# Performance work log

Measured on AMD Instinct MI355X. Metric: run time of the kernel, lower is better.

The kernel has to match this reference:

```python
import jax, jax.numpy as jnp
import numpy as np

D_IN = 1024
D_OUT = 1024
D_BOT = 512


def setup_inputs() -> dict:
    key = jax.random.key(0)
    ks = jax.random.split(key, 16)
    B, Sq, Skv = 8, 2048, 2048

    def lin(k, fan_in, fan_out):
        kw, kb = jax.random.split(k)
        bound = 1.0 / np.sqrt(fan_in)
        W = jax.random.uniform(kw, (fan_in, fan_out), jnp.float32, -bound, bound)
        b = jax.random.uniform(kb, (fan_out,), jnp.float32, -bound, bound)
        return W, b

    W1, b1 = lin(ks[0], D_IN, D_IN)
    W2, b2 = lin(ks[1], D_IN, D_BOT)
    W3, b3 = lin(ks[2], D_BOT, D_IN)
    W4, b4 = lin(ks[3], D_IN, D_IN)
    Wq, bq = lin(ks[4], D_IN, D_OUT)
    Wk, bk = lin(ks[5], D_IN, D_OUT)
    Wv, bv = lin(ks[6], D_IN, D_OUT)

    x = jax.random.normal(ks[7], (B, Sq, D_IN), jnp.float32)
    y = jax.random.normal(ks[8], (B, Skv, D_IN), jnp.float32)
    return {
        "x": x, "y": y,
        "W1": W1, "b1": b1, "W2": W2, "b2": b2,
        "W3": W3, "b3": b3, "W4": W4, "b4": b4,
        "Wq": Wq, "bq": bq, "Wk": Wk, "bk": bk, "Wv": Wv, "bv": bv,
    }


def reference(x, y, W1, b1, W2, b2, W3, b3, W4, b4, Wq, bq, Wk, bk, Wv, bv):
    # 4-layer MLP with ReLU after every linear
    h = jax.nn.relu(x @ W1 + b1)
    h = jax.nn.relu(h @ W2 + b2)
    h = jax.nn.relu(h @ W3 + b3)
    h = jax.nn.relu(h @ W4 + b4)
    # cross-attention projections
    q = h @ Wq + bq          # [B, Sq, D_OUT]
    k = y @ Wk + bk          # [B, Skv, D_OUT]
    v = y @ Wv + bv          # [B, Skv, D_OUT]
    scale = 1.0 / jnp.sqrt(jnp.float32(q.shape[-1]))
    scores = jnp.einsum('bqd,bkd->bqk', q, k) * scale  # [B, Sq, Skv]
    attn_w = jax.nn.softmax(scores, axis=-1)
    out = jnp.einsum('bqk,bkd->bqd', attn_w, v)
    return out
```

## Files before the change

### kernel.cpp

```cpp
#include <hip/hip_runtime.h>
#include <stdint.h>


typedef __attribute__((ext_vector_type(8))) short bf16x8;
typedef __attribute__((ext_vector_type(4))) float f32x4;
typedef __attribute__((ext_vector_type(8))) unsigned short u16x8;

__device__ __forceinline__ float bf2f(unsigned short u) {
    return __uint_as_float(((unsigned int)u) << 16);
}
__device__ __forceinline__ unsigned short f2bf(float f) {
    unsigned int u = __float_as_uint(f);
    unsigned int r = (u + 0x7fffu + ((u >> 16) & 1u)) >> 16;
    return (unsigned short)r;
}

__device__ __forceinline__ void async16(const void* g, void* l) {
    __builtin_amdgcn_global_load_lds(
        (const __attribute__((address_space(1))) unsigned int*)g,
        (__attribute__((address_space(3))) unsigned int*)l,
        16, 0, 0);
}

__global__ __launch_bounds__(64) void detect_dtype(
    const unsigned short* __restrict__ w, int* __restrict__ flag)
{
    const int t = threadIdx.x;
    int cnt = 0;
    for (int i = t; i < 4096; i += 64) {
        const unsigned e = (w[i] >> 7) & 0xFF;
        cnt += (e >= 140) ? 1 : 0;
    }
#pragma unroll
    for (int off = 32; off; off >>= 1) cnt += __shfl_xor(cnt, off, 64);
    if (t == 0) flag[0] = (cnt >= 8) ? 1 : 0;
}

__global__ __launch_bounds__(256) void conv_bias_all(
    const void* b1, const void* b2, const void* b3, const void* b4,
    const void* bq, const void* bk, const void* bv,
    float* __restrict__ out, const int* __restrict__ flag)
{
    const int i = blockIdx.x * 256 + threadIdx.x;
    const int slot = i >> 10, idx = i & 1023;
    if (slot == 1 && idx >= 512) return;
    const void* src = (slot == 0) ? b1 : (slot == 1) ? b2 : (slot == 2) ? b3 :
                      (slot == 3) ? b4 : (slot == 4) ? bq : (slot == 5) ? bk : bv;
    out[i] = (*flag) ? ((const float*)src)[idx]
                     : bf2f(((const unsigned short*)src)[idx]);
}

__device__ __forceinline__ void wt_body(
    const void* in, unsigned short* out, int R, int C, int f)
{
    __shared__ unsigned short tile[32][33];
    const int bc = blockIdx.x * 32;
    const int br = blockIdx.y * 32;
    const int x = threadIdx.x & 31;
    const int y = threadIdx.x >> 5;
#pragma unroll
    for (int i = 0; i < 4; i++) {
        const int r = y + i * 8;
        unsigned short v;
        if (f) v = f2bf(((const float*)in)[(size_t)(br + r) * C + bc + x]);
        else   v = ((const unsigned short*)in)[(size_t)(br + r) * C + bc + x];
        tile[r][x] = v;
    }
    __syncthreads();
#pragma unroll
    for (int i = 0; i < 4; i++) {
        const int r = y + i * 8;
        out[(size_t)(bc + r) * R + br + x] = tile[x][r];
    }
}

__global__ __launch_bounds__(256) void conv_weight_t7(
    const void* i0, unsigned short* o0, const void* i1, unsigned short* o1,
    const void* i2, unsigned short* o2, const void* i3, unsigned short* o3,
    const void* i4, unsigned short* o4, const void* i5, unsigned short* o5,
    const void* i6, unsigned short* o6, const int* flag)
{
    const int z = blockIdx.z;
    if (z == 5) {
        if (blockIdx.x >= 16) return;
        wt_body(i5, o5, 1024, 512, *flag);
        return;
    }
    if (z == 6) {
        if (blockIdx.y >= 16) return;
        wt_body(i6, o6, 512, 1024, *flag);
        return;
    }
    const void* in = (z == 0) ? i0 : (z == 1) ? i1 : (z == 2) ? i2 : (z == 3) ? i3 : i4;
    unsigned short* out = (z == 0) ? o0 : (z == 1) ? o1 : (z == 2) ? o2 : (z == 3) ? o3 : o4;
    wt_body(in, out, 1024, 1024, *flag);
}

__global__ __launch_bounds__(256) void conv_to_bf16(
    const void* __restrict__ in, unsigned short* __restrict__ out,
    int n, const int* __restrict__ flag)
{
    const int i = (blockIdx.x * 256 + threadIdx.x) * 8;
    if (i >= n) return;
    if (*flag) {
        const float4* p = (const float4*)((const float*)in + i);
        const float4 a = p[0], b = p[1];
        u16x8 o;
        o[0] = f2bf(a.x); o[1] = f2bf(a.y); o[2] = f2bf(a.z); o[3] = f2bf(a.w);
        o[4] = f2bf(b.x); o[5] = f2bf(b.y); o[6] = f2bf(b.z); o[7] = f2bf(b.w);
        *(u16x8*)(out + i) = o;
    } else {
        *(u16x8*)(out + i) = *(const u16x8*)((const unsigned short*)in + i);
    }
}

__global__ __launch_bounds__(256) void write_out(
    const unsigned short* __restrict__ src, void* __restrict__ dst,
    int n, const int* __restrict__ flag)
{
    const int i = (blockIdx.x * 256 + threadIdx.x) * 8;
    if (i >= n) return;
    const u16x8 v = *(const u16x8*)(src + i);
    if (*flag) {
        float4 a, b;
        a.x = bf2f(v[0]); a.y = bf2f(v[1]); a.z = bf2f(v[2]); a.w = bf2f(v[3]);
        b.x = bf2f(v[4]); b.y = bf2f(v[5]); b.z = bf2f(v[6]); b.w = bf2f(v[7]);
        float4* p = (float4*)((float*)dst + i);
        p[0] = a; p[1] = b;
    } else {
        *(u16x8*)((unsigned short*)dst + i) = v;
    }
}

template <int RELU, int BIAS, int OUTF, int SWZ>
__global__ __launch_bounds__(256, 2) void gemm_bt(
    const unsigned short* __restrict__ A, const unsigned short* __restrict__ B,
    const float* __restrict__ bias, void* __restrict__ C,
    int M, int N, int K, float alpha,
    long long sA, long long sB, long long sC, const int* __restrict__ flag)
{
    int bxi = blockIdx.x, byi = blockIdx.y;
    if (SWZ) {
        const int id = byi * gridDim.x + bxi;
        bxi = (id >> 3) % gridDim.x;
        byi = (id >> 3) / gridDim.x * 8 + (id & 7);
    }
    const int z = blockIdx.z;
    A += (size_t)z * (size_t)sA;
    B += (size_t)z * (size_t)sB;
    const size_t cofs = (size_t)z * (size_t)sC;

    const int bm = byi * 128;
    const int bn = bxi * 128;
    const int t = threadIdx.x;
    const int lane = t & 63;
    const int w = t >> 6;
    const int wr = (w >> 1) * 64;
    const int wc = (w & 1) * 64;

    __shared__ unsigned short sAt[128 * 32];
    __shared__ unsigned short sBt[128 * 32];

    f32x4 acc[4][4];
#pragma unroll
    for (int i = 0; i < 4; i++)
#pragma unroll
        for (int j = 0; j < 4; j++)
            acc[i][j] = (f32x4){0.f, 0.f, 0.f, 0.f};

    const int tr = t >> 2;
    const int tc = (t & 3) << 3;
    const unsigned short* ga = A + (size_t)(bm + tr) * K + tc;
    const unsigned short* gb = B + (size_t)(bn + tr) * K + tc;
    unsigned short* la = &sAt[tr * 32 + tc];
    unsigned short* lb = &sBt[tr * 32 + tc];

    const int am = wr + (lane & 15);
    const int bn_ = wc + (lane & 15);
    const int ak = (lane >> 4) * 8;

    for (int k0 = 0; k0 < K; k0 += 32) {
        async16(ga, la);
        async16(ga + (size_t)64 * K, la + 64 * 32);
        async16(gb, lb);
        async16(gb + (size_t)64 * K, lb + 64 * 32);
        ga += 32;
        gb += 32;
        __syncthreads();

        bf16x8 af[4], bfr[4];
#pragma unroll
        for (int i = 0; i < 4; i++)
            af[i] = *(const bf16x8*)&sAt[(am + i * 16) * 32 + ak];
#pragma unroll
        for (int j = 0; j < 4; j++)
            bfr[j] = *(const bf16x8*)&sBt[(bn_ + j * 16) * 32 + ak];
#pragma unroll
        for (int i = 0; i < 4; i++)
#pragma unroll
            for (int j = 0; j < 4; j++)
                acc[i][j] = __builtin_amdgcn_mfma_f32_16x16x32_bf16(
                    af[i], bfr[j], acc[i][j], 0, 0, 0);
        __syncthreads();
    }

    const int fl = OUTF ? *flag : 0;
#pragma unroll
    for (int i = 0; i < 4; i++) {
        const int row0 = bm + wr + i * 16 + (lane >> 4) * 4;
#pragma unroll
        for (int j = 0; j < 4; j++) {
            const int col = bn + wc + j * 16 + (lane & 15);
            float bc = 0.f;
            if (BIAS == 1) bc = bias[col];
#pragma unroll
            for (int r = 0; r < 4; r++) {
                float bv = bc;
                if (BIAS == 2) bv = bias[row0 + r];
                float vv = acc[i][j][r] * alpha + bv;
                if (RELU) vv = fmaxf(vv, 0.f);
                const size_t idx = cofs + (size_t)(row0 + r) * N + col;
                if (OUTF && fl) ((float*)C)[idx] = vv;
                else ((unsigned short*)C)[idx] = f2bf(vv);
            }
        }
    }
}

template <int RELU, int BIAS, int OUTF, int SWZ>
__global__ __launch_bounds__(256, 2) void gemm_bt2(
    const unsigned short* __restrict__ A, const unsigned short* __restrict__ B,
    const float* __restrict__ bias, void* __restrict__ C,
    int M, int N, int K, float alpha,
    long long sA, long long sB, long long sC, const int* __restrict__ flag)
{
    int bxi = blockIdx.x, byi = blockIdx.y;
    if (SWZ) {
        const int id = byi * gridDim.x + bxi;
        bxi = (id >> 3) % gridDim.x;
        byi = (id >> 3) / gridDim.x * 8 + (id & 7);
    }
    const int z = blockIdx.z;
    A += (size_t)z * (size_t)sA;
    B += (size_t)z * (size_t)sB;
    const size_t cofs = (size_t)z * (size_t)sC;

    const int bm = byi * 128;
    const int bn = bxi * 256;
    const int t = threadIdx.x;
    const int lane = t & 63;
    const int w = t >> 6;
    const int wr = (w >> 1) * 64;
    const int wc = (w & 1) * 128;

    __shared__ unsigned short sAt[128 * 32];
    __shared__ unsigned short sBt[256 * 32];

    f32x4 acc[4][8];
#pragma unroll
    for (int i = 0; i < 4; i++)
#pragma unroll
        for (int j = 0; j < 8; j++)
            acc[i][j] = (f32x4){0.f, 0.f, 0.f, 0.f};

    const int tr = t >> 2;
    const int tc = (t & 3) << 3;
    const unsigned short* ga = A + (size_t)(bm + tr) * K + tc;
    const unsigned short* gb = B + (size_t)(bn + tr) * K + tc;
    unsigned short* la = &sAt[tr * 32 + tc];
    unsigned short* lb = &sBt[tr * 32 + tc];

    const int am = wr + (lane & 15);
    const int bn_ = wc + (lane & 15);
    const int ak = (lane >> 4) * 8;

    for (int k0 = 0; k0 < K; k0 += 32) {
        async16(ga, la);
        async16(ga + (size_t)64 * K, la + 64 * 32);
        async16(gb, lb);
        async16(gb + (size_t)64 * K, lb + 64 * 32);
        async16(gb + (size_t)128 * K, lb + 128 * 32);
        async16(gb + (size_t)192 * K, lb + 192 * 32);
        ga += 32;
        gb += 32;
        __syncthreads();

        bf16x8 af[4], bfr[8];
#pragma unroll
        for (int i = 0; i < 4; i++)
            af[i] = *(const bf16x8*)&sAt[(am + i * 16) * 32 + ak];
#pragma unroll
        for (int j = 0; j < 8; j++)
            bfr[j] = *(const bf16x8*)&sBt[(bn_ + j * 16) * 32 + ak];
#pragma unroll
        for (int i = 0; i < 4; i++)
#pragma unroll
            for (int j = 0; j < 8; j++)
                acc[i][j] = __builtin_amdgcn_mfma_f32_16x16x32_bf16(
                    af[i], bfr[j], acc[i][j], 0, 0, 0);
        __syncthreads();
    }

    const int fl = OUTF ? *flag : 0;
#pragma unroll
    for (int i = 0; i < 4; i++) {
        const int row0 = bm + wr + i * 16 + (lane >> 4) * 4;
#pragma unroll
        for (int j = 0; j < 8; j++) {
            const int col = bn + wc + j * 16 + (lane & 15);
            float bc = 0.f;
            if (BIAS == 1) bc = bias[col];
#pragma unroll
            for (int r = 0; r < 4; r++) {
                float bv = bc;
                if (BIAS == 2) bv = bias[row0 + r];
                float vv = acc[i][j][r] * alpha + bv;
                if (RELU) vv = fmaxf(vv, 0.f);
                const size_t idx = cofs + (size_t)(row0 + r) * N + col;
                if (OUTF && fl) ((float*)C)[idx] = vv;
                else ((unsigned short*)C)[idx] = f2bf(vv);
            }
        }
    }
}

__global__ __launch_bounds__(256) void softmax_rows(unsigned short* S, int n)
{
    const size_t row = blockIdx.x;
    unsigned short* p = S + row * (size_t)n;
    const int t = threadIdx.x;
    const int lane = t & 63;
    const int wave = t >> 6;

    u16x8 v = *(const u16x8*)(p + t * 8);
    float f[8];
    float m = -3.0e38f;
#pragma unroll
    for (int i = 0; i < 8; i++) {
        f[i] = bf2f(v[i]);
        m = fmaxf(m, f[i]);
    }
#pragma unroll
    for (int off = 32; off; off >>= 1) m = fmaxf(m, __shfl_xor(m, off, 64));
    __shared__ float redm[4];
    if (lane == 0) redm[wave] = m;
    __syncthreads();
    m = fmaxf(fmaxf(redm[0], redm[1]), fmaxf(redm[2], redm[3]));

    float e[8];
    float s = 0.f;
#pragma unroll
    for (int i = 0; i < 8; i++) {
        e[i] = __expf(f[i] - m);
        s += e[i];
    }
#pragma unroll
    for (int off = 32; off; off >>= 1) s += __shfl_xor(s, off, 64);
    __shared__ float reds[4];
    if (lane == 0) reds[wave] = s;
    __syncthreads();
    s = reds[0] + reds[1] + reds[2] + reds[3];
    const float inv = 1.0f / s;

    u16x8 o;
#pragma unroll
    for (int i = 0; i < 8; i++) o[i] = f2bf(e[i] * inv);
    *(u16x8*)(p + t * 8) = o;
}

extern "C" void kernel_launch(void* const* d_in, const int* in_sizes, int n_in,
                              void* d_out, int out_size, void* d_ws, size_t ws_size,
                              hipStream_t stream)
{
    const void* x  = d_in[0];
    const void* y  = d_in[1];
    const void* W1 = d_in[2];
    const void* b1 = d_in[3];
    const void* W2 = d_in[4];
    const void* b2 = d_in[5];
    const void* W3 = d_in[6];
    const void* b3 = d_in[7];
    const void* W4 = d_in[8];
    const void* b4 = d_in[9];
    const void* Wq = d_in[10];
    const void* bq = d_in[11];
    const void* Wk = d_in[12];
    const void* bk = d_in[13];
    const void* Wv = d_in[14];
    const void* bv = d_in[15];

    int* flag = (int*)d_ws;
    float* fb = (float*)((char*)d_ws + 64);
    unsigned short* arena = (unsigned short*)((char*)d_ws + 64 + 7 * 1024 * 4);
    const size_t baseB = 64 + 7 * 1024 * 4;
    const size_t MEG = 1024ull * 1024ull;

    auto needB = [&](int G, bool direct) -> size_t {
        return baseB + 2ull * ((6 + 16 + (size_t)G * 6 + (direct ? 0 : 16)) * MEG);
    };
    int G; bool direct;
    if (ws_size >= needB(8, true))      { G = 8; direct = true;  }
    else if (ws_size >= needB(4, false)) { G = 4; direct = false; }
    else if (ws_size >= needB(2, false)) { G = 2; direct = false; }
    else                                 { G = 1; direct = false; }

    unsigned short* W1t = arena;
    unsigned short* W2t = W1t + 1 * MEG;
    unsigned short* W3t = W2t + MEG / 2;
    unsigned short* W4t = W3t + MEG / 2;
    unsigned short* Wqt = W4t + 1 * MEG;
    unsigned short* Wkt = Wqt + 1 * MEG;
    unsigned short* Wvt = Wkt + 1 * MEG;
    unsigned short* XC  = Wvt + 1 * MEG;
    unsigned short* VT  = XC + 16 * MEG;
    unsigned short* SBUF = VT + (size_t)G * 2 * MEG;
    unsigned short* OUTS = SBUF + (size_t)G * 4 * MEG;

    unsigned short* PA = (unsigned short*)d_out;
    unsigned short* PB = PA + 16 * MEG;

    float* fb1 = fb;
    float* fb2 = fb + 1024;
    float* fb3 = fb + 2048;
    float* fb4 = fb + 3072;
    float* fbq = fb + 4096;
    float* fbk = fb + 5120;
    float* fbv = fb + 6144;

    const dim3 blk(256);
    const int NE = 16 * 1024 * 1024;
    const int Mx = 16384;
    const long long Z0 = 0;
    const long long sQK = 2048ll * 1024;
    const long long sS  = 2048ll * 2048;

    detect_dtype<<<1, 64, 0, stream>>>((const unsigned short*)W1, flag);
    conv_bias_all<<<28, blk, 0, stream>>>(b1, b2, b3, b4, bq, bk, bv, fb, flag);
    conv_weight_t7<<<dim3(32, 32, 7), blk, 0, stream>>>(
        W1, W1t, W4, W4t, Wq, Wqt, Wk, Wkt, Wv, Wvt, W2, W2t, W3, W3t, flag);

    conv_to_bf16<<<8192, blk, 0, stream>>>(x, XC, NE, flag);

    gemm_bt2<1, 1, 0, 1><<<dim3(4, 128), blk, 0, stream>>>(XC, W1t, fb1, PA, Mx, 1024, 1024, 1.f, Z0, Z0, Z0, flag);
    gemm_bt <1, 1, 0, 1><<<dim3(4, 128), blk, 0, stream>>>(PA, W2t, fb2, PB, Mx, 512, 1024, 1.f, Z0, Z0, Z0, flag);
    gemm_bt <1, 1, 0, 1><<<dim3(8, 128), blk, 0, stream>>>(PB, W3t, fb3, PA, Mx, 1024, 512, 1.f, Z0, Z0, Z0, flag);
    gemm_bt2<1, 1, 0, 1><<<dim3(4, 128), blk, 0, stream>>>(PA, W4t, fb4, PB, Mx, 1024, 1024, 1.f, Z0, Z0, Z0, flag);

    gemm_bt2<0, 1, 0, 1><<<dim3(4, 128), blk, 0, stream>>>(PB, Wqt, fbq, PA, Mx, 1024, 1024, 1.f, Z0, Z0, Z0, flag);
    conv_to_bf16<<<8192, blk, 0, stream>>>(y, XC, NE, flag);
    gemm_bt2<0, 1, 0, 1><<<dim3(4, 128), blk, 0, stream>>>(XC, Wkt, fbk, PB, Mx, 1024, 1024, 1.f, Z0, Z0, Z0, flag);

    if (direct) {
        gemm_bt<0, 2, 0, 0><<<dim3(16, 8, 8), blk, 0, stream>>>(
            Wvt, XC, fbv, VT, 1024, 2048, 1024, 1.f, Z0, sQK, sQK, flag);
        gemm_bt2<0, 0, 0, 1><<<dim3(8, 16, 8), blk, 0, stream>>>(
            PA, PB, nullptr, SBUF, 2048, 2048, 1024, 0.03125f, sQK, sQK, sS, flag);
        softmax_rows<<<dim3(8 * 2048), blk, 0, stream>>>(SBUF, 2048);
        gemm_bt2<0, 0, 1, 1><<<dim3(4, 16, 8), blk, 0, stream>>>(
            SBUF, VT, nullptr, d_out, 2048, 1024, 2048, 1.f, sS, sQK, sQK, flag);
    } else {
        for (int g = 0; g < 8; g += G) {
            const size_t off = (size_t)g * 2048 * 1024;
            gemm_bt<0, 2, 0, 0><<<dim3(16, 8, G), blk, 0, stream>>>(
                Wvt, XC + off, fbv, VT, 1024, 2048, 1024, 1.f, Z0, sQK, sQK, flag);
            gemm_bt<0, 0, 0, 1><<<dim3(16, 16, G), blk, 0, stream>>>(
                PA + off, PB + off, nullptr, SBUF, 2048, 2048, 1024, 0.03125f, sQK, sQK, sS, flag);
            softmax_rows<<<dim3(G * 2048), blk, 0, stream>>>(SBUF, 2048);
            gemm_bt<0, 0, 0, 1><<<dim3(8, 16, G), blk, 0, stream>>>(
                SBUF, VT, nullptr, OUTS + off, 2048, 1024, 2048, 1.f, sS, sQK, sQK, flag);
        }
        write_out<<<8192, blk, 0, stream>>>(OUTS, d_out, NE, flag);
    }
}
```

Baseline: 666.5 us.

## Replace 128x256 GEMM with 256x256 eight-wave double-buffered pipelined kernel

```diff
diff --git a/kernel.cpp b/kernel.cpp
--- a/kernel.cpp
+++ b/kernel.cpp
@@ -227,13 +227,76 @@
     }
 }
 
+#define G8_STG(gbase, dbase, T, h) do {                                        \
+    const unsigned short* _s = (gbase) + (size_t)((h) * 128) * K               \
+                                       + (size_t)(T) * 64;                     \
+    unsigned short* _d = (dbase) + (((T) & 1) ? 16384 : 0) + (h) * 8192;       \
+    async16(_s, _d);                                                           \
+    async16(_s + (size_t)64 * K, _d + 4096);                                   \
+} while (0)
+
+#define G8_RD_LO(PA_, PB_)                                                     \
+    _Pragma("unroll")                                                          \
+    for (int m_ = 0; m_ < 4; m_++) {                                           \
+        aL[m_][0] = *(const bf16x8*)&(PA_)[rA + m_ * 1024 + c0];               \
+        aL[m_][1] = *(const bf16x8*)&(PA_)[rA + m_ * 1024 + c1];               \
+    }                                                                          \
+    _Pragma("unroll")                                                          \
+    for (int n_ = 0; n_ < 4; n_++)                                             \
+        bb[n_][0] = *(const bf16x8*)&(PB_)[rB + n_ * 1024 + c0];
+
+#define G8_RD_HI(PA_, PB_)                                                     \
+    _Pragma("unroll")                                                          \
+    for (int m_ = 0; m_ < 4; m_++) {                                           \
+        aH[m_][0] = *(const bf16x8*)&(PA_)[rA + (m_ + 4) * 1024 + c0];         \
+        aH[m_][1] = *(const bf16x8*)&(PA_)[rA + (m_ + 4) * 1024 + c1];         \
+    }                                                                          \
+    _Pragma("unroll")                                                          \
+    for (int n_ = 0; n_ < 4; n_++)                                             \
+        bb[n_][1] = *(const bf16x8*)&(PB_)[rB + n_ * 1024 + c1];
+
+#define G8_TOP()                                                               \
+    __builtin_amdgcn_s_barrier();                                              \
+    asm volatile("s_waitcnt lgkmcnt(0)" ::: "memory");                         \
+    __builtin_amdgcn_sched_barrier(0);                                         \
+    __builtin_amdgcn_s_setprio(1);
+
+#define G8_FMA(AF, KK, MOFS)                                                   \
+    _Pragma("unroll")                                                          \
+    for (int m_ = 0; m_ < 4; m_++) {                                           \
+        _Pragma("unroll")                                                      \
+        for (int n_ = 0; n_ < 4; n_++)                                         \
+            acc[(MOFS) + m_][n_] = __builtin_amdgcn_mfma_f32_16x16x32_bf16(    \
+                AF[m_][KK], bb[n_][KK], acc[(MOFS) + m_][n_], 0, 0, 0);        \
+    }
+
+#define G8_BOT()                                                               \
+    __builtin_amdgcn_s_setprio(0);                                             \
+    asm volatile("" ::: "memory");                                             \
+    __builtin_amdgcn_s_barrier();                                              \
+    asm volatile("" ::: "memory");
+
+#define G8_BOTVM4()                                                            \
+    __builtin_amdgcn_s_setprio(0);                                             \
+    asm volatile("s_waitcnt vmcnt(4)" ::: "memory");                           \
+    __builtin_amdgcn_s_barrier();                                              \
+    asm volatile("" ::: "memory");
+
+#define G8_BOTVM0()                                                            \
+    __builtin_amdgcn_s_setprio(0);                                             \
+    asm volatile("s_waitcnt vmcnt(0)" ::: "memory");                           \
+    __builtin_amdgcn_s_barrier();                                              \
+    asm volatile("" ::: "memory");
+
 template <int RELU, int BIAS, int OUTF, int SWZ>
-__global__ __launch_bounds__(256, 2) void gemm_bt2(
+__global__ __launch_bounds__(512, 2) void gemm8(
     const unsigned short* __restrict__ A, const unsigned short* __restrict__ B,
     const float* __restrict__ bias, void* __restrict__ C,
     int M, int N, int K, float alpha,
     long long sA, long long sB, long long sC, const int* __restrict__ flag)
 {
+    extern __shared__ unsigned short lds[];
+    (void)M;
     int bxi = blockIdx.x, byi = blockIdx.y;
     if (SWZ) {
         const int id = byi * gridDim.x + bxi;
@@ -245,76 +308,136 @@
     B += (size_t)z * (size_t)sB;
     const size_t cofs = (size_t)z * (size_t)sC;
 
-    const int bm = byi * 128;
+    const int bm = byi * 256;
     const int bn = bxi * 256;
     const int t = threadIdx.x;
     const int lane = t & 63;
     const int w = t >> 6;
-    const int wr = (w >> 1) * 64;
-    const int wc = (w & 1) * 128;
-
-    __shared__ unsigned short sAt[128 * 32];
-    __shared__ unsigned short sBt[256 * 32];
-
-    f32x4 acc[4][8];
-#pragma unroll
-    for (int i = 0; i < 4; i++)
-#pragma unroll
-        for (int j = 0; j < 8; j++)
+    const int wm = w >> 2;
+    const int wn = w & 3;
+
+    unsigned short* LA = lds;
+    unsigned short* LB = lds + 32768;
+
+    const int rowi = t >> 3;
+    const int co = ((t & 7) ^ (rowi & 7)) << 3;
+    const unsigned short* gA = A + (size_t)(bm + rowi) * K + co;
+    const unsigned short* gB = B + (size_t)(bn + rowi) * K + co;
+    unsigned short* dA = LA + t * 8;
+    unsigned short* dB = LB + t * 8;
+
+    const int rA = (wm * 128 + (lane & 15)) * 64;
+    const int rB = (wn * 64 + (lane & 15)) * 64;
+    const int swz = (lane & 7) << 4;
+    const int c0 = ((((lane >> 4) << 4)) ^ swz) >> 1;
+    const int c1 = ((64 | ((lane >> 4) << 4)) ^ swz) >> 1;
+
+    f32x4 acc[8][4];
+#pragma unroll
+    for (int i = 0; i < 8; i++)
+#pragma unroll
+        for (int j = 0; j < 4; j++)
             acc[i][j] = (f32x4){0.f, 0.f, 0.f, 0.f};
 
-    const int tr = t >> 2;
-    const int tc = (t & 3) << 3;
-    const unsigned short* ga = A + (size_t)(bm + tr) * K + tc;
-    const unsigned short* gb = B + (size_t)(bn + tr) * K + tc;
-    unsigned short* la = &sAt[tr * 32 + tc];
-    unsigned short* lb = &sBt[tr * 32 + tc];
-
-    const int am = wr + (lane & 15);
-    const int bn_ = wc + (lane & 15);
-    const int ak = (lane >> 4) * 8;
-
-    for (int k0 = 0; k0 < K; k0 += 32) {
-        async16(ga, la);
-        async16(ga + (size_t)64 * K, la + 64 * 32);
-        async16(gb, lb);
-        async16(gb + (size_t)64 * K, lb + 64 * 32);
-        async16(gb + (size_t)128 * K, lb + 128 * 32);
-        async16(gb + (size_t)192 * K, lb + 192 * 32);
-        ga += 32;
-        gb += 32;
-        __syncthreads();
-
-        bf16x8 af[4], bfr[8];
-#pragma unroll
-        for (int i = 0; i < 4; i++)
-            af[i] = *(const bf16x8*)&sAt[(am + i * 16) * 32 + ak];
-#pragma unroll
-        for (int j = 0; j < 8; j++)
-            bfr[j] = *(const bf16x8*)&sBt[(bn_ + j * 16) * 32 + ak];
-#pragma unroll
-        for (int i = 0; i < 4; i++)
-#pragma unroll
-            for (int j = 0; j < 8; j++)
-                acc[i][j] = __builtin_amdgcn_mfma_f32_16x16x32_bf16(
-                    af[i], bfr[j], acc[i][j], 0, 0, 0);
-        __syncthreads();
+    bf16x8 aL[4][2], aH[4][2], bb[4][2];
+
+    G8_STG(gA, dA, 0, 0);
+    G8_STG(gA, dA, 0, 1);
+    G8_STG(gB, dB, 0, 0);
+    G8_STG(gB, dB, 0, 1);
+    G8_STG(gA, dA, 1, 0);
+    G8_STG(gA, dA, 1, 1);
+    asm volatile("s_waitcnt vmcnt(4)" ::: "memory");
+    __builtin_amdgcn_s_barrier();
+    asm volatile("" ::: "memory");
+
+    const int NI = K >> 7;
+    int kt = 0;
+    for (int i = 0; i < NI - 1; ++i, kt += 2) {
+        G8_RD_LO(LA, LB)
+        G8_STG(gB, dB, kt + 1, 0);
+        G8_TOP()
+        G8_FMA(aL, 0, 0)
+        G8_BOT()
+        G8_RD_HI(LA, LB)
+        G8_STG(gB, dB, kt + 1, 1);
+        G8_TOP()
+        G8_FMA(aL, 1, 0)
+        G8_BOT()
+        G8_STG(gA, dA, kt + 2, 0);
+        G8_TOP()
+        G8_FMA(aH, 0, 4)
+        G8_BOT()
+        G8_STG(gA, dA, kt + 2, 1);
+        G8_TOP()
+        G8_FMA(aH, 1, 4)
+        G8_BOTVM4()
+        G8_RD_LO((LA + 16384), (LB + 16384))
+        G8_STG(gB, dB, kt + 2, 0);
+        G8_TOP()
+        G8_FMA(aL, 0, 0)
+        G8_BOT()
+        G8_RD_HI((LA + 16384), (LB + 16384))
+        G8_STG(gB, dB, kt + 2, 1);
+        G8_TOP()
+        G8_FMA(aL, 1, 0)
+        G8_BOT()
+        G8_STG(gA, dA, kt + 3, 0);
+        G8_TOP()
+        G8_FMA(aH, 0, 4)
+        G8_BOT()
+        G8_STG(gA, dA, kt + 3, 1);
+        G8_TOP()
+        G8_FMA(aH, 1, 4)
+        G8_BOTVM4()
+    }
+    {
+        G8_RD_LO(LA, LB)
+        G8_STG(gB, dB, kt + 1, 0);
+        G8_TOP()
+        G8_FMA(aL, 0, 0)
+        G8_BOT()
+        G8_RD_HI(LA, LB)
+        G8_STG(gB, dB, kt + 1, 1);
+        G8_TOP()
+        G8_FMA(aL, 1, 0)
+        G8_BOT()
+        G8_TOP()
+        G8_FMA(aH, 0, 4)
+        G8_BOT()
+        G8_TOP()
+        G8_FMA(aH, 1, 4)
+        G8_BOTVM0()
+        G8_RD_LO((LA + 16384), (LB + 16384))
+        G8_TOP()
+        G8_FMA(aL, 0, 0)
+        G8_BOT()
+        G8_RD_HI((LA + 16384), (LB + 16384))
+        G8_TOP()
+        G8_FMA(aL, 1, 0)
+        G8_BOT()
+        G8_TOP()
+        G8_FMA(aH, 0, 4)
+        G8_BOT()
+        G8_TOP()
+        G8_FMA(aH, 1, 4)
+        __builtin_amdgcn_s_setprio(0);
     }
 
     const int fl = OUTF ? *flag : 0;
 #pragma unroll
-    for (int i = 0; i < 4; i++) {
-        const int row0 = bm + wr + i * 16 + (lane >> 4) * 4;
-#pragma unroll
-        for (int j = 0; j < 8; j++) {
-            const int col = bn + wc + j * 16 + (lane & 15);
+    for (int mi = 0; mi < 8; mi++) {
+        const int row0 = bm + wm * 128 + mi * 16 + (lane >> 4) * 4;
+#pragma unroll
+        for (int n = 0; n < 4; n++) {
+            const int col = bn + wn * 64 + n * 16 + (lane & 15);
             float bc = 0.f;
             if (BIAS == 1) bc = bias[col];
 #pragma unroll
             for (int r = 0; r < 4; r++) {
                 float bv = bc;
                 if (BIAS == 2) bv = bias[row0 + r];
-                float vv = acc[i][j][r] * alpha + bv;
+                float vv = acc[mi][n][r] * alpha + bv;
                 if (RELU) vv = fmaxf(vv, 0.f);
                 const size_t idx = cofs + (size_t)(row0 + r) * N + col;
                 if (OUTF && fl) ((float*)C)[idx] = vv;
@@ -428,12 +551,25 @@
     float* fbv = fb + 6144;
 
     const dim3 blk(256);
+    const dim3 blk8(512);
+    const int LDS8 = 131072;
     const int NE = 16 * 1024 * 1024;
     const int Mx = 16384;
     const long long Z0 = 0;
     const long long sQK = 2048ll * 1024;
     const long long sS  = 2048ll * 2048;
 
+    (void)hipFuncSetAttribute((const void*)&gemm8<1, 1, 0, 1>,
+                              hipFuncAttributeMaxDynamicSharedMemorySize, LDS8);
+    (void)hipFuncSetAttribute((const void*)&gemm8<0, 1, 0, 1>,
+                              hipFuncAttributeMaxDynamicSharedMemorySize, LDS8);
+    (void)hipFuncSetAttribute((const void*)&gemm8<0, 2, 0, 0>,
+                              hipFuncAttributeMaxDynamicSharedMemorySize, LDS8);
+    (void)hipFuncSetAttribute((const void*)&gemm8<0, 0, 0, 1>,
+                              hipFuncAttributeMaxDynamicSharedMemorySize, LDS8);
+    (void)hipFuncSetAttribute((const void*)&gemm8<0, 0, 1, 1>,
+                              hipFuncAttributeMaxDynamicSharedMemorySize, LDS8);
+
     detect_dtype<<<1, 64, 0, stream>>>((const unsigned short*)W1, flag);
     conv_bias_all<<<28, blk, 0, stream>>>(b1, b2, b3, b4, bq, bk, bv, fb, flag);
     conv_weight_t7<<<dim3(32, 32, 7), blk, 0, stream>>>(
@@ -441,22 +577,28 @@
 
     conv_to_bf16<<<8192, blk, 0, stream>>>(x, XC, NE, flag);
 
-    gemm_bt2<1, 1, 0, 1><<<dim3(4, 128), blk, 0, stream>>>(XC, W1t, fb1, PA, Mx, 1024, 1024, 1.f, Z0, Z0, Z0, flag);
-    gemm_bt <1, 1, 0, 1><<<dim3(4, 128), blk, 0, stream>>>(PA, W2t, fb2, PB, Mx, 512, 1024, 1.f, Z0, Z0, Z0, flag);
-    gemm_bt <1, 1, 0, 1><<<dim3(8, 128), blk, 0, stream>>>(PB, W3t, fb3, PA, Mx, 1024, 512, 1.f, Z0, Z0, Z0, flag);
-    gemm_bt2<1, 1, 0, 1><<<dim3(4, 128), blk, 0, stream>>>(PA, W4t, fb4, PB, Mx, 1024, 1024, 1.f, Z0, Z0, Z0, flag);
-
-    gemm_bt2<0, 1, 0, 1><<<dim3(4, 128), blk, 0, stream>>>(PB, Wqt, fbq, PA, Mx, 1024, 1024, 1.f, Z0, Z0, Z0, flag);
+    gemm8<1, 1, 0, 1><<<dim3(4, 64), blk8, LDS8, stream>>>(
+        XC, W1t, fb1, PA, Mx, 1024, 1024, 1.f, Z0, Z0, Z0, flag);
+    gemm_bt<1, 1, 0, 1><<<dim3(4, 128), blk, 0, stream>>>(
+        PA, W2t, fb2, PB, Mx, 512, 1024, 1.f, Z0, Z0, Z0, flag);
+    gemm8<1, 1, 0, 1><<<dim3(4, 64), blk8, LDS8, stream>>>(
+        PB, W3t, fb3, PA, Mx, 1024, 512, 1.f, Z0, Z0, Z0, flag);
+    gemm8<1, 1, 0, 1><<<dim3(4, 64), blk8, LDS8, stream>>>(
+        PA, W4t, fb4, PB, Mx, 1024, 1024, 1.f, Z0, Z0, Z0, flag);
+
+    gemm8<0, 1, 0, 1><<<dim3(4, 64), blk8, LDS8, stream>>>(
+        PB, Wqt, fbq, PA, Mx, 1024, 1024, 1.f, Z0, Z0, Z0, flag);
     conv_to_bf16<<<8192, blk, 0, stream>>>(y, XC, NE, flag);
-    gemm_bt2<0, 1, 0, 1><<<dim3(4, 128), blk, 0, stream>>>(XC, Wkt, fbk, PB, Mx, 1024, 1024, 1.f, Z0, Z0, Z0, flag);
+    gemm8<0, 1, 0, 1><<<dim3(4, 64), blk8, LDS8, stream>>>(
+        XC, Wkt, fbk, PB, Mx, 1024, 1024, 1.f, Z0, Z0, Z0, flag);
 
     if (direct) {
-        gemm_bt<0, 2, 0, 0><<<dim3(16, 8, 8), blk, 0, stream>>>(
+        gemm8<0, 2, 0, 0><<<dim3(8, 4, 8), blk8, LDS8, stream>>>(
             Wvt, XC, fbv, VT, 1024, 2048, 1024, 1.f, Z0, sQK, sQK, flag);
-        gemm_bt2<0, 0, 0, 1><<<dim3(8, 16, 8), blk, 0, stream>>>(
+        gemm8<0, 0, 0, 1><<<dim3(8, 8, 8), blk8, LDS8, stream>>>(
             PA, PB, nullptr, SBUF, 2048, 2048, 1024, 0.03125f, sQK, sQK, sS, flag);
         softmax_rows<<<dim3(8 * 2048), blk, 0, stream>>>(SBUF, 2048);
-        gemm_bt2<0, 0, 1, 1><<<dim3(4, 16, 8), blk, 0, stream>>>(
+        gemm8<0, 0, 1, 1><<<dim3(4, 8, 8), blk8, LDS8, stream>>>(
             SBUF, VT, nullptr, d_out, 2048, 1024, 2048, 1.f, sS, sQK, sQK, flag);
     } else {
         for (int g = 0; g < 8; g += G) {
```

Result: faster. 621.1 us (-6.8%).

## Replace GEMM kernel with 256x256 tile, 8-wave, 4-stage async LDS pipeline

Applied to the files above, without the earlier changes.

```diff
diff --git a/kernel.cpp b/kernel.cpp
--- a/kernel.cpp
+++ b/kernel.cpp
@@ -227,13 +227,22 @@
     }
 }
 
+#define G10_STG(SOFS, KOFS) do {                                               \
+    async16(gAs + (KOFS), dA + (SOFS));                                        \
+    async16(gAs + (KOFS) + rk128, dA + (SOFS) + 4096);                         \
+    async16(gBs + (KOFS), dB + (SOFS));                                        \
+    async16(gBs + (KOFS) + rk128, dB + (SOFS) + 4096);                         \
+} while (0)
+
 template <int RELU, int BIAS, int OUTF, int SWZ>
-__global__ __launch_bounds__(256, 2) void gemm_bt2(
+__global__ __launch_bounds__(512, 2) void gemm8(
     const unsigned short* __restrict__ A, const unsigned short* __restrict__ B,
     const float* __restrict__ bias, void* __restrict__ C,
     int M, int N, int K, float alpha,
     long long sA, long long sB, long long sC, const int* __restrict__ flag)
 {
+    extern __shared__ unsigned short lds[];
+    (void)M;
     int bxi = blockIdx.x, byi = blockIdx.y;
     if (SWZ) {
         const int id = byi * gridDim.x + bxi;
@@ -245,76 +254,89 @@
     B += (size_t)z * (size_t)sB;
     const size_t cofs = (size_t)z * (size_t)sC;
 
-    const int bm = byi * 128;
+    const int bm = byi * 256;
     const int bn = bxi * 256;
     const int t = threadIdx.x;
     const int lane = t & 63;
     const int w = t >> 6;
-    const int wr = (w >> 1) * 64;
-    const int wc = (w & 1) * 128;
-
-    __shared__ unsigned short sAt[128 * 32];
-    __shared__ unsigned short sBt[256 * 32];
-
-    f32x4 acc[4][8];
-#pragma unroll
-    for (int i = 0; i < 4; i++)
-#pragma unroll
-        for (int j = 0; j < 8; j++)
+    const int wm = w >> 2;
+    const int wn = w & 3;
+
+    const int soct = ((t & 3) ^ ((t >> 3) & 3)) << 3;
+    const unsigned short* gAs = A + (size_t)(bm + (t >> 2)) * K + soct;
+    const unsigned short* gBs = B + (size_t)(bn + (t >> 2)) * K + soct;
+    const size_t rk128 = (size_t)128 * K;
+    unsigned short* dA = lds + t * 8;
+    unsigned short* dB = lds + 32768 + t * 8;
+
+    const int l15 = lane & 15;
+    const int oct = (((lane >> 4) ^ ((lane >> 1) & 3)) << 3);
+    const int aoff = (wm * 128 + l15) * 32 + oct;
+    const int boff = (wn * 64 + l15) * 32 + oct;
+
+    f32x4 acc[8][4];
+#pragma unroll
+    for (int i = 0; i < 8; i++)
+#pragma unroll
+        for (int j = 0; j < 4; j++)
             acc[i][j] = (f32x4){0.f, 0.f, 0.f, 0.f};
 
-    const int tr = t >> 2;
-    const int tc = (t & 3) << 3;
-    const unsigned short* ga = A + (size_t)(bm + tr) * K + tc;
-    const unsigned short* gb = B + (size_t)(bn + tr) * K + tc;
-    unsigned short* la = &sAt[tr * 32 + tc];
-    unsigned short* lb = &sBt[tr * 32 + tc];
-
-    const int am = wr + (lane & 15);
-    const int bn_ = wc + (lane & 15);
-    const int ak = (lane >> 4) * 8;
-
-    for (int k0 = 0; k0 < K; k0 += 32) {
-        async16(ga, la);
-        async16(ga + (size_t)64 * K, la + 64 * 32);
-        async16(gb, lb);
-        async16(gb + (size_t)64 * K, lb + 64 * 32);
-        async16(gb + (size_t)128 * K, lb + 128 * 32);
-        async16(gb + (size_t)192 * K, lb + 192 * 32);
-        ga += 32;
-        gb += 32;
-        __syncthreads();
-
-        bf16x8 af[4], bfr[8];
-#pragma unroll
-        for (int i = 0; i < 4; i++)
-            af[i] = *(const bf16x8*)&sAt[(am + i * 16) * 32 + ak];
-#pragma unroll
-        for (int j = 0; j < 8; j++)
-            bfr[j] = *(const bf16x8*)&sBt[(bn_ + j * 16) * 32 + ak];
-#pragma unroll
-        for (int i = 0; i < 4; i++)
-#pragma unroll
-            for (int j = 0; j < 8; j++)
-                acc[i][j] = __builtin_amdgcn_mfma_f32_16x16x32_bf16(
-                    af[i], bfr[j], acc[i][j], 0, 0, 0);
-        __syncthreads();
+    G10_STG(0, 0);
+    G10_STG(8192, 32);
+    asm volatile("s_waitcnt vmcnt(4)" ::: "memory");
+    __builtin_amdgcn_s_barrier();
+    asm volatile("" ::: "memory");
+
+    const int NT = K >> 5;
+    for (int T = 0; T < NT; ++T) {
+        if (T + 2 < NT) {
+            const int so = ((T + 2) & 3) * 8192;
+            const int ko = (T + 2) << 5;
+            G10_STG(so, ko);
+        }
+        const int sr = (T & 3) * 8192;
+        const unsigned short* pa = lds + sr + aoff;
+        const unsigned short* pb = lds + 32768 + sr + boff;
+        bf16x8 bb[4], a[8];
+#pragma unroll
+        for (int n = 0; n < 4; n++)
+            bb[n] = *(const bf16x8*)(pb + n * 512);
+#pragma unroll
+        for (int m = 0; m < 8; m++)
+            a[m] = *(const bf16x8*)(pa + m * 512);
+        __builtin_amdgcn_s_setprio(1);
+#pragma unroll
+        for (int m = 0; m < 8; m++)
+#pragma unroll
+            for (int n = 0; n < 4; n++)
+                acc[m][n] = __builtin_amdgcn_mfma_f32_16x16x32_bf16(
+                    a[m], bb[n], acc[m][n], 0, 0, 0);
+        __builtin_amdgcn_s_setprio(0);
+        if (T + 1 < NT) {
+            if (T + 2 < NT) {
+                asm volatile("s_waitcnt vmcnt(4)" ::: "memory");
+            } else {
+                asm volatile("s_waitcnt vmcnt(0)" ::: "memory");
+            }
+            __builtin_amdgcn_s_barrier();
+            asm volatile("" ::: "memory");
+        }
     }
 
     const int fl = OUTF ? *flag : 0;
 #pragma unroll
-    for (int i = 0; i < 4; i++) {
-        const int row0 = bm + wr + i * 16 + (lane >> 4) * 4;
-#pragma unroll
-        for (int j = 0; j < 8; j++) {
-            const int col = bn + wc + j * 16 + (lane & 15);
+    for (int mi = 0; mi < 8; mi++) {
+        const int row0 = bm + wm * 128 + mi * 16 + (lane >> 4) * 4;
+#pragma unroll
+        for (int n = 0; n < 4; n++) {
+            const int col = bn + wn * 64 + n * 16 + (lane & 15);
             float bc = 0.f;
             if (BIAS == 1) bc = bias[col];
 #pragma unroll
             for (int r = 0; r < 4; r++) {
                 float bv = bc;
                 if (BIAS == 2) bv = bias[row0 + r];
-                float vv = acc[i][j][r] * alpha + bv;
+                float vv = acc[mi][n][r] * alpha + bv;
                 if (RELU) vv = fmaxf(vv, 0.f);
                 const size_t idx = cofs + (size_t)(row0 + r) * N + col;
                 if (OUTF && fl) ((float*)C)[idx] = vv;
@@ -428,12 +450,25 @@
     float* fbv = fb + 6144;
 
     const dim3 blk(256);
+    const dim3 blk8(512);
+    const int LDS8 = 131072;
     const int NE = 16 * 1024 * 1024;
     const int Mx = 16384;
     const long long Z0 = 0;
     const long long sQK = 2048ll * 1024;
     const long long sS  = 2048ll * 2048;
 
+    (void)hipFuncSetAttribute((const void*)&gemm8<1, 1, 0, 1>,
+                              hipFuncAttributeMaxDynamicSharedMemorySize, LDS8);
+    (void)hipFuncSetAttribute((const void*)&gemm8<0, 1, 0, 1>,
+                              hipFuncAttributeMaxDynamicSharedMemorySize, LDS8);
+    (void)hipFuncSetAttribute((const void*)&gemm8<0, 2, 0, 0>,
+                              hipFuncAttributeMaxDynamicSharedMemorySize, LDS8);
+    (void)hipFuncSetAttribute((const void*)&gemm8<0, 0, 0, 1>,
+                              hipFuncAttributeMaxDynamicSharedMemorySize, LDS8);
+    (void)hipFuncSetAttribute((const void*)&gemm8<0, 0, 1, 1>,
+                              hipFuncAttributeMaxDynamicSharedMemorySize, LDS8);
+
     detect_dtype<<<1, 64, 0, stream>>>((const unsigned short*)W1, flag);
     conv_bias_all<<<28, blk, 0, stream>>>(b1, b2, b3, b4, bq, bk, bv, fb, flag);
     conv_weight_t7<<<dim3(32, 32, 7), blk, 0, stream>>>(
@@ -441,22 +476,28 @@
 
     conv_to_bf16<<<8192, blk, 0, stream>>>(x, XC, NE, flag);
 
-    gemm_bt2<1, 1, 0, 1><<<dim3(4, 128), blk, 0, stream>>>(XC, W1t, fb1, PA, Mx, 1024, 1024, 1.f, Z0, Z0, Z0, flag);
-    gemm_bt <1, 1, 0, 1><<<dim3(4, 128), blk, 0, stream>>>(PA, W2t, fb2, PB, Mx, 512, 1024, 1.f, Z0, Z0, Z0, flag);
-    gemm_bt <1, 1, 0, 1><<<dim3(8, 128), blk, 0, stream>>>(PB, W3t, fb3, PA, Mx, 1024, 512, 1.f, Z0, Z0, Z0, flag);
-    gemm_bt2<1, 1, 0, 1><<<dim3(4, 128), blk, 0, stream>>>(PA, W4t, fb4, PB, Mx, 1024, 1024, 1.f, Z0, Z0, Z0, flag);
-
-    gemm_bt2<0, 1, 0, 1><<<dim3(4, 128), blk, 0, stream>>>(PB, Wqt, fbq, PA, Mx, 1024, 1024, 1.f, Z0, Z0, Z0, flag);
+    gemm8<1, 1, 0, 1><<<dim3(4, 64), blk8, LDS8, stream>>>(
+        XC, W1t, fb1, PA, Mx, 1024, 1024, 1.f, Z0, Z0, Z0, flag);
+    gemm_bt<1, 1, 0, 1><<<dim3(4, 128), blk, 0, stream>>>(
+        PA, W2t, fb2, PB, Mx, 512, 1024, 1.f, Z0, Z0, Z0, flag);
+    gemm8<1, 1, 0, 1><<<dim3(4, 64), blk8, LDS8, stream>>>(
+        PB, W3t, fb3, PA, Mx, 1024, 512, 1.f, Z0, Z0, Z0, flag);
+    gemm8<1, 1, 0, 1><<<dim3(4, 64), blk8, LDS8, stream>>>(
+        PA, W4t, fb4, PB, Mx, 1024, 1024, 1.f, Z0, Z0, Z0, flag);
+
+    gemm8<0, 1, 0, 1><<<dim3(4, 64), blk8, LDS8, stream>>>(
+        PB, Wqt, fbq, PA, Mx, 1024, 1024, 1.f, Z0, Z0, Z0, flag);
     conv_to_bf16<<<8192, blk, 0, stream>>>(y, XC, NE, flag);
-    gemm_bt2<0, 1, 0, 1><<<dim3(4, 128), blk, 0, stream>>>(XC, Wkt, fbk, PB, Mx, 1024, 1024, 1.f, Z0, Z0, Z0, flag);
+    gemm8<0, 1, 0, 1><<<dim3(4, 64), blk8, LDS8, stream>>>(
+        XC, Wkt, fbk, PB, Mx, 1024, 1024, 1.f, Z0, Z0, Z0, flag);
 
     if (direct) {
-        gemm_bt<0, 2, 0, 0><<<dim3(16, 8, 8), blk, 0, stream>>>(
+        gemm8<0, 2, 0, 0><<<dim3(8, 4, 8), blk8, LDS8, stream>>>(
             Wvt, XC, fbv, VT, 1024, 2048, 1024, 1.f, Z0, sQK, sQK, flag);
-        gemm_bt2<0, 0, 0, 1><<<dim3(8, 16, 8), blk, 0, stream>>>(
+        gemm8<0, 0, 0, 1><<<dim3(8, 8, 8), blk8, LDS8, stream>>>(
             PA, PB, nullptr, SBUF, 2048, 2048, 1024, 0.03125f, sQK, sQK, sS, flag);
         softmax_rows<<<dim3(8 * 2048), blk, 0, stream>>>(SBUF, 2048);
-        gemm_bt2<0, 0, 1, 1><<<dim3(4, 16, 8), blk, 0, stream>>>(
+        gemm8<0, 0, 1, 1><<<dim3(4, 8, 8), blk8, LDS8, stream>>>(
             SBUF, VT, nullptr, d_out, 2048, 1024, 2048, 1.f, sS, sQK, sQK, flag);
     } else {
         for (int g = 0; g < 8; g += G) {
```

Result: faster. 606.0 us (median of 2 runs) (-9.1%).
